# Kernel optimization log

Measured on AMD Instinct MI355X. Metric: run time of the kernel, lower is better.

Reference implementation:

```python
import jax, jax.numpy as jnp
import numpy as np

DT = 0.025    # ms, integration time step
CM = 1.0      # uF/cm^2 membrane capacitance
E_NA, E_K, E_L = 50.0, -77.0, -54.387  # mV reversal potentials

T, N = 8192, 2048


def setup_inputs() -> dict:
    key = jax.random.key(0)
    ks = jax.random.split(key, 5)
    return {
        "input_estim": 5.0 * jax.random.normal(ks[0], (T, N), dtype=jnp.float32),  # uA/cm^2 stim per segment per step
        "V0": -65.0 + 2.0 * jax.random.normal(ks[1], (N,), dtype=jnp.float32),
        "m0": 0.05 + 0.02 * jax.random.uniform(ks[2], (N,), dtype=jnp.float32),
        "h0": 0.60 + 0.05 * jax.random.uniform(ks[3], (N,), dtype=jnp.float32),
        "n0": 0.32 + 0.05 * jax.random.uniform(ks[4], (N,), dtype=jnp.float32),
        "g_na": 120.0 * jnp.ones((N,), jnp.float32),
        "g_k": 36.0 * jnp.ones((N,), jnp.float32),
        "g_l": 0.3 * jnp.ones((N,), jnp.float32),
        "g_ax": 5.0 * jnp.ones((N,), jnp.float32),  # axial coupling conductance between neighbor segments
    }


def _rates(V):
    am = 0.1 * (V + 40.0) / (1.0 - jnp.exp(-(V + 40.0) / 10.0))
    bm = 4.0 * jnp.exp(-(V + 65.0) / 18.0)
    ah = 0.07 * jnp.exp(-(V + 65.0) / 20.0)
    bh = 1.0 / (1.0 + jnp.exp(-(V + 35.0) / 10.0))
    an = 0.01 * (V + 55.0) / (1.0 - jnp.exp(-(V + 55.0) / 10.0))
    bn = 0.125 * jnp.exp(-(V + 65.0) / 80.0)
    return am, bm, ah, bh, an, bn


def reference(input_estim, V0, m0, h0, n0, g_na, g_k, g_l, g_ax):
    def step(state, i_stim):
        V, m, h, n = state
        am, bm, ah, bh, an, bn = _rates(V)
        i_ion = (g_na * m**3 * h * (V - E_NA)
                 + g_k * n**4 * (V - E_K)
                 + g_l * (V - E_L))
        # sealed-end cable: zero-flux boundaries via edge padding
        Vp = jnp.pad(V, (1, 1), mode="edge")
        i_ax = g_ax * (Vp[:-2] + Vp[2:] - 2.0 * V)
        dV = (i_ax + i_stim - i_ion) / CM
        # total transmembrane current (capacitive + ionic) = axial + stim
        mem_cur = CM * dV + i_ion
        new_state = (V + DT * dV,
                     m + DT * (am * (1.0 - m) - bm * m),
                     h + DT * (ah * (1.0 - h) - bh * h),
                     n + DT * (an * (1.0 - n) - bn * n))
        return new_state, (mem_cur, V)

    state0 = (V0, m0, h0, n0)
    (Vf, mf, hf, nf), (mem_currents, mem_voltages) = jax.lax.scan(step, state0, input_estim)
    # (mem_currents_over_time, mem_voltage_over_time, final state)
    return mem_currents, mem_voltages, Vf, mf, hf, nf
```

## Files before the change

### kernel.cpp

```cpp
#include <hip/hip_runtime.h>

typedef unsigned long long u64;
typedef unsigned int u32;

#define TSTEPS 8192
#define NSEG   2048
#define DTC    0.025f

#define KST    28
#define KTAIL  16
#define WAVE   64
#define COWN   8
#define NBLK   (NSEG / COWN)
#define NPH    ((TSTEPS + KST - 1) / KST)
#define JLO    KST
#define LDP    66

constexpr double L2E = 1.4426950408889634074;

#define AM_A ((float)(-0.1 * L2E))
#define CEM  0.018315638888734179f
#define CEH  0.030197383422318501f
#define CEN  0.0040867714384640666f
#define BM_A ((float)(-L2E / 18.0))
#define BM_B ((float)(2.0 - 65.0 * L2E / 18.0))
#define QA   ((float)(-L2E / 80.0))
#define QB   ((float)(-65.0 * L2E / 80.0))
#define CAH  0.2645751311064591f

#define AL(p) __hip_atomic_load((p), __ATOMIC_RELAXED, __HIP_MEMORY_SCOPE_AGENT)
#define AS(p, v) __hip_atomic_store((p), (v), __ATOMIC_RELAXED, __HIP_MEMORY_SCOPE_AGENT)

__device__ __forceinline__ u64 pack_tag(float v, int tag) {
    return ((u64)(u32)tag << 32) | (u64)__float_as_uint(v);
}
__device__ __forceinline__ float lo_f(u64 w) { return __uint_as_float((u32)w); }
__device__ __forceinline__ float bperm(int addr, float v) {
    return __int_as_float(__builtin_amdgcn_ds_bpermute(addr, __float_as_int(v)));
}

__device__ __forceinline__ void rates(float V, float& am, float& bm,
                                      float& ah, float& bh,
                                      float& an, float& bn)
{
    const float em0 = __builtin_amdgcn_exp2f(V * AM_A);
    am = __builtin_fmaf(0.1f, V, 4.0f) *
         __builtin_amdgcn_rcpf(__builtin_fmaf(-CEM, em0, 1.0f));
    an = __builtin_fmaf(0.01f, V, 0.55f) *
         __builtin_amdgcn_rcpf(__builtin_fmaf(-CEN, em0, 1.0f));
    bh = __builtin_amdgcn_rcpf(__builtin_fmaf(CEH, em0, 1.0f));
    bm = __builtin_amdgcn_exp2f(__builtin_fmaf(V, BM_A, BM_B));
    const float q = __builtin_amdgcn_exp2f(__builtin_fmaf(V, QA, QB));
    const float tq = CAH * (q * q);
    ah = tq * tq;
    bn = 0.125f * q;
}

template <int KS>
__device__ __forceinline__ void run_phase(
    int p, int b, int j, int s, int sc,
    bool owned, int addrL, int addrR,
    float gna, float gk, float gl, float gax,
    const float* __restrict__ stim, u64* __restrict__ tstate,
    float* __restrict__ out_cur, float* __restrict__ out_volt,
    float* lds, float& V, float& m, float& h, float& n, bool pub)
{
    const int t0 = p * KST;
    const float* sp = stim + (size_t)t0 * NSEG + sc;

    float st[KS];
#pragma unroll
    for (int k = 0; k < KS; ++k)
        st[k] = sp[(size_t)k * NSEG];
    __builtin_amdgcn_sched_barrier(0);

    const bool needLoad = (!owned) || (p == 0);
    const u64* sb = tstate + (size_t)(p & 1) * 4 * NSEG + sc;
    {
        u64 w0 = 0, w1 = 0, w2 = 0, w3 = 0;
        int ok;
        do {
            ok = 1;
            if (needLoad) {
                w0 = AL(sb);            w1 = AL(sb + NSEG);
                w2 = AL(sb + 2 * NSEG); w3 = AL(sb + 3 * NSEG);
                ok = (int)(w0 >> 32) >= p && (int)(w1 >> 32) >= p &&
                     (int)(w2 >> 32) >= p && (int)(w3 >> 32) >= p;
            }
        } while (!__all(ok));
        if (needLoad) {
            V = lo_f(w0); m = lo_f(w1); h = lo_f(w2); n = lo_f(w3);
        }
    }

    float Vl = bperm(addrL, V);
    float Vr = bperm(addrR, V);
    float am, bm, ah, bh, an, bn;
    rates(V, am, bm, ah, bh, an, bn);

    float2* ld2 = (float2*)lds;
#pragma unroll
    for (int k = 0; k < KS; ++k) {
        const float is = st[k];
        const float ax = (Vl + Vr) - 2.0f * V;
        const float mc = __builtin_fmaf(gax, ax, is);
        const float m3 = m * m * m;
        const float n2 = n * n;
        const float i_ion = gna * m3 * h * (V - 50.0f)
                          + gk * (n2 * n2) * (V + 77.0f)
                          + gl * (V + 54.387f);
        const float dV = mc - i_ion;
        const float Vn = __builtin_fmaf(DTC, dV, V);
        const float VlN = bperm(addrL, Vn);
        const float VrN = bperm(addrR, Vn);

        ld2[k * LDP + j] = make_float2(mc, V);

        float amN, bmN, ahN, bhN, anN, bnN;
        rates(Vn, amN, bmN, ahN, bhN, anN, bnN);

        m = __builtin_fmaf(DTC, __builtin_fmaf(-(am + bm), m, am), m);
        h = __builtin_fmaf(DTC, __builtin_fmaf(-(ah + bh), h, ah), h);
        n = __builtin_fmaf(DTC, __builtin_fmaf(-(an + bn), n, an), n);

        V = Vn; Vl = VlN; Vr = VrN;
        am = amN; bm = bmN; ah = ahN; bh = bhN; an = anN; bn = bnN;
    }

    if (pub && owned) {
        u64* pb = tstate + (size_t)((p + 1) & 1) * 4 * NSEG + s;
        AS(pb,            pack_tag(V, p + 1));
        AS(pb + NSEG,     pack_tag(m, p + 1));
        AS(pb + 2 * NSEG, pack_tag(h, p + 1));
        AS(pb + 3 * NSEG, pack_tag(n, p + 1));
    }
    __builtin_amdgcn_sched_barrier(0);

    const int sbase = b * COWN;
#pragma unroll
    for (int base = 0; base < KS * COWN; base += WAVE) {
        const int idx = base + j;
        if (idx < KS * COWN) {
            const int t  = idx >> 3;
            const int sl = idx & 7;
            const float* lp = lds + (size_t)(t * LDP + JLO + sl) * 2;
            const size_t go = (size_t)(t0 + t) * NSEG + (sbase + sl);
            __builtin_nontemporal_store(lp[0], out_cur + go);
            __builtin_nontemporal_store(lp[1], out_volt + go);
        }
    }
}

__global__ __launch_bounds__(WAVE, 1) void hh_persist(
    const float* __restrict__ stim,
    const float* __restrict__ gna_p, const float* __restrict__ gk_p,
    const float* __restrict__ gl_p,  const float* __restrict__ gax_p,
    u64* __restrict__ tstate,
    float* __restrict__ out_cur, float* __restrict__ out_volt,
    float* __restrict__ tail)
{
    const int j = threadIdx.x;
    const int b = blockIdx.x;
    const int s = b * COWN - KST + j;
    const int sc = s < 0 ? 0 : (s > NSEG - 1 ? NSEG - 1 : s);
    const bool owned = (j >= JLO) && (j < JLO + COWN);

    const int jl = (s <= 0)        ? j : (j > 0  ? j - 1 : 0);
    const int jr = (s >= NSEG - 1) ? j : (j < 63 ? j + 1 : 63);
    const int addrL = jl * 4;
    const int addrR = jr * 4;

    const float gna = gna_p[sc], gk = gk_p[sc], gl = gl_p[sc], gax = gax_p[sc];

    __shared__ float lds[KST * LDP * 2];

    float V = 0.f, m = 0.f, h = 0.f, n = 0.f;

    for (int p = 0; p < NPH - 1; ++p)
        run_phase<KST>(p, b, j, s, sc, owned, addrL, addrR, gna, gk, gl, gax,
                       stim, tstate, out_cur, out_volt, lds, V, m, h, n, true);
    run_phase<KTAIL>(NPH - 1, b, j, s, sc, owned, addrL, addrR, gna, gk, gl, gax,
                     stim, tstate, out_cur, out_volt, lds, V, m, h, n, false);

    if (owned) {
        tail[s] = V; tail[NSEG + s] = m;
        tail[2 * NSEG + s] = h; tail[3 * NSEG + s] = n;
    }
}

__global__ void hh_init(const float* __restrict__ V0, const float* __restrict__ m0,
                        const float* __restrict__ h0, const float* __restrict__ n0,
                        u64* __restrict__ tstate)
{
    const int i = blockIdx.x * blockDim.x + threadIdx.x;
    if (i < NSEG) {
        tstate[i]            = pack_tag(V0[i], 0);
        tstate[NSEG + i]     = pack_tag(m0[i], 0);
        tstate[2 * NSEG + i] = pack_tag(h0[i], 0);
        tstate[3 * NSEG + i] = pack_tag(n0[i], 0);
        u64* b1 = tstate + 4 * NSEG;
        const u64 inv = (u64)(u32)0x80000000u << 32;
        b1[i] = inv; b1[NSEG + i] = inv; b1[2 * NSEG + i] = inv; b1[3 * NSEG + i] = inv;
    }
}

extern "C" void kernel_launch(void* const* d_in, const int* in_sizes, int n_in,
                              void* d_out, int out_size, void* d_ws, size_t ws_size,
                              hipStream_t stream)
{
    const float* stim = (const float*)d_in[0];
    const float* V0   = (const float*)d_in[1];
    const float* m0   = (const float*)d_in[2];
    const float* h0   = (const float*)d_in[3];
    const float* n0   = (const float*)d_in[4];
    const float* gna  = (const float*)d_in[5];
    const float* gk   = (const float*)d_in[6];
    const float* gl   = (const float*)d_in[7];
    const float* gax  = (const float*)d_in[8];

    float* out      = (float*)d_out;
    float* out_cur  = out;
    float* out_volt = out + (size_t)TSTEPS * NSEG;
    float* tail     = out + 2 * (size_t)TSTEPS * NSEG;

    u64* tstate = (u64*)d_ws;

    hipLaunchKernelGGL(hh_init, dim3(8), dim3(256), 0, stream,
                       V0, m0, h0, n0, tstate);
    hipLaunchKernelGGL(hh_persist, dim3(NBLK), dim3(WAVE), 0, stream,
                       stim, gna, gk, gl, gax, tstate,
                       out_cur, out_volt, tail);
}
```

Measured before the change: 1.164 ms.

## Split halo window across two waves coupled by per-step LDS ring exchange

New measurement: 2.317 ms. 1.99x slower.

```diff
diff --git a/kernel.cpp b/kernel.cpp
--- a/kernel.cpp
+++ b/kernel.cpp
@@ -7,14 +7,15 @@
 #define NSEG   2048
 #define DTC    0.025f
 
-#define KST    28
+#define KST    56
 #define KTAIL  16
+#define NT     128
 #define WAVE   64
-#define COWN   8
+#define COWN   16
 #define NBLK   (NSEG / COWN)
-#define NPH    ((TSTEPS + KST - 1) / KST)
-#define JLO    KST
-#define LDP    66
+#define NPH    147
+#define JLO    56
+#define RING   4
 
 constexpr double L2E = 1.4426950408889634074;
 
@@ -30,6 +31,8 @@
 
 #define AL(p) __hip_atomic_load((p), __ATOMIC_RELAXED, __HIP_MEMORY_SCOPE_AGENT)
 #define AS(p, v) __hip_atomic_store((p), (v), __ATOMIC_RELAXED, __HIP_MEMORY_SCOPE_AGENT)
+#define LDSL(p) __hip_atomic_load((p), __ATOMIC_RELAXED, __HIP_MEMORY_SCOPE_WORKGROUP)
+#define LDSS(p, v) __hip_atomic_store((p), (v), __ATOMIC_RELAXED, __HIP_MEMORY_SCOPE_WORKGROUP)
 
 __device__ __forceinline__ u64 pack_tag(float v, int tag) {
     return ((u64)(u32)tag << 32) | (u64)__float_as_uint(v);
@@ -58,14 +61,16 @@
 
 template <int KS>
 __device__ __forceinline__ void run_phase(
-    int p, int b, int j, int s, int sc,
-    bool owned, int addrL, int addrR,
+    int p, int b, int tid, int j, int s, int sc,
+    bool owned, bool edge, bool le, bool re, int addrL, int addrR,
     float gna, float gk, float gl, float gax,
+    u64* ringMe, u64* ringOt,
     const float* __restrict__ stim, u64* __restrict__ tstate,
     float* __restrict__ out_cur, float* __restrict__ out_volt,
-    float* lds, float& V, float& m, float& h, float& n, bool pub)
+    float2* lbuf, float& V, float& m, float& h, float& n, bool pub)
 {
     const int t0 = p * KST;
+    const int g0 = t0;
     const float* sp = stim + (size_t)t0 * NSEG + sc;
 
     float st[KS];
@@ -93,14 +98,28 @@
         }
     }
 
+    if (edge) LDSS(ringMe + (g0 & (RING - 1)), pack_tag(V, g0 + 1));
     float Vl = bperm(addrL, V);
     float Vr = bperm(addrR, V);
+    {
+        u64 w = 0; int ok;
+        do {
+            ok = 1;
+            if (edge) {
+                w = LDSL(ringOt + (g0 & (RING - 1)));
+                ok = (int)(w >> 32) >= g0 + 1;
+            }
+        } while (!__all(ok));
+        if (edge) { if (tid == 63) Vr = lo_f(w); else Vl = lo_f(w); }
+    }
+    Vl = le ? V : Vl;
+    Vr = re ? V : Vr;
     float am, bm, ah, bh, an, bn;
     rates(V, am, bm, ah, bh, an, bn);
 
-    float2* ld2 = (float2*)lds;
 #pragma unroll
     for (int k = 0; k < KS; ++k) {
+        const int G = g0 + k;
         const float is = st[k];
         const float ax = (Vl + Vr) - 2.0f * V;
         const float mc = __builtin_fmaf(gax, ax, is);
@@ -111,10 +130,11 @@
                           + gl * (V + 54.387f);
         const float dV = mc - i_ion;
         const float Vn = __builtin_fmaf(DTC, dV, V);
-        const float VlN = bperm(addrL, Vn);
-        const float VrN = bperm(addrR, Vn);
-
-        ld2[k * LDP + j] = make_float2(mc, V);
+        if (edge) LDSS(ringMe + ((G + 1) & (RING - 1)), pack_tag(Vn, G + 2));
+        float VlN = bperm(addrL, Vn);
+        float VrN = bperm(addrR, Vn);
+
+        if (owned) lbuf[k * 8 + (tid & 7)] = make_float2(mc, V);
 
         float amN, bmN, ahN, bhN, anN, bnN;
         rates(Vn, amN, bmN, ahN, bhN, anN, bnN);
@@ -122,6 +142,20 @@
         m = __builtin_fmaf(DTC, __builtin_fmaf(-(am + bm), m, am), m);
         h = __builtin_fmaf(DTC, __builtin_fmaf(-(ah + bh), h, ah), h);
         n = __builtin_fmaf(DTC, __builtin_fmaf(-(an + bn), n, an), n);
+
+        {
+            u64 w = 0; int ok;
+            do {
+                ok = 1;
+                if (edge) {
+                    w = LDSL(ringOt + ((G + 1) & (RING - 1)));
+                    ok = (int)(w >> 32) >= G + 2;
+                }
+            } while (!__all(ok));
+            if (edge) { if (tid == 63) VrN = lo_f(w); else VlN = lo_f(w); }
+        }
+        VlN = le ? Vn : VlN;
+        VrN = re ? Vn : VrN;
 
         V = Vn; Vl = VlN; Vr = VrN;
         am = amN; bm = bmN; ah = ahN; bh = bhN; an = anN; bn = bnN;
@@ -136,22 +170,20 @@
     }
     __builtin_amdgcn_sched_barrier(0);
 
-    const int sbase = b * COWN;
+    const int sbase = b * COWN + ((tid >= WAVE) ? 8 : 0);
 #pragma unroll
-    for (int base = 0; base < KS * COWN; base += WAVE) {
+    for (int base = 0; base < KS * 8; base += WAVE) {
         const int idx = base + j;
-        if (idx < KS * COWN) {
-            const int t  = idx >> 3;
-            const int sl = idx & 7;
-            const float* lp = lds + (size_t)(t * LDP + JLO + sl) * 2;
-            const size_t go = (size_t)(t0 + t) * NSEG + (sbase + sl);
-            __builtin_nontemporal_store(lp[0], out_cur + go);
-            __builtin_nontemporal_store(lp[1], out_volt + go);
+        if (idx < KS * 8) {
+            const float2 v = lbuf[idx];
+            const size_t go = (size_t)(t0 + (idx >> 3)) * NSEG + sbase + (idx & 7);
+            __builtin_nontemporal_store(v.x, out_cur + go);
+            __builtin_nontemporal_store(v.y, out_volt + go);
         }
     }
 }
 
-__global__ __launch_bounds__(WAVE, 1) void hh_persist(
+__global__ __launch_bounds__(NT, 1) void hh_persist(
     const float* __restrict__ stim,
     const float* __restrict__ gna_p, const float* __restrict__ gk_p,
     const float* __restrict__ gl_p,  const float* __restrict__ gax_p,
@@ -159,28 +191,39 @@
     float* __restrict__ out_cur, float* __restrict__ out_volt,
     float* __restrict__ tail)
 {
-    const int j = threadIdx.x;
-    const int b = blockIdx.x;
-    const int s = b * COWN - KST + j;
-    const int sc = s < 0 ? 0 : (s > NSEG - 1 ? NSEG - 1 : s);
-    const bool owned = (j >= JLO) && (j < JLO + COWN);
-
-    const int jl = (s <= 0)        ? j : (j > 0  ? j - 1 : 0);
-    const int jr = (s >= NSEG - 1) ? j : (j < 63 ? j + 1 : 63);
-    const int addrL = jl * 4;
-    const int addrR = jr * 4;
+    const int tid = threadIdx.x;
+    const int j   = tid & 63;
+    const int b   = blockIdx.x;
+    const int s   = b * COWN - KST + tid;
+    const int sc  = s < 0 ? 0 : (s > NSEG - 1 ? NSEG - 1 : s);
+    const bool owned = (tid >= JLO) && (tid < JLO + COWN);
+    const bool edge  = (tid == 63) || (tid == 64);
+    const bool le = (s <= 0);
+    const bool re = (s >= NSEG - 1);
+
+    const int addrL = (j > 0  ? j - 1 : j) * 4;
+    const int addrR = (j < 63 ? j + 1 : j) * 4;
 
     const float gna = gna_p[sc], gk = gk_p[sc], gl = gl_p[sc], gax = gax_p[sc];
 
-    __shared__ float lds[KST * LDP * 2];
+    __shared__ u64 ring[2][RING];
+    __shared__ float2 lb0[KST * 8], lb1[KST * 8];
+    float2* lbuf = (tid < WAVE) ? lb0 : lb1;
+    u64* ringMe = (tid == 63) ? ring[0] : ring[1];
+    u64* ringOt = (tid == 63) ? ring[1] : ring[0];
+
+    if (tid < 2 * RING) ((u64*)ring)[tid] = 0;
+    __syncthreads();
 
     float V = 0.f, m = 0.f, h = 0.f, n = 0.f;
 
     for (int p = 0; p < NPH - 1; ++p)
-        run_phase<KST>(p, b, j, s, sc, owned, addrL, addrR, gna, gk, gl, gax,
-                       stim, tstate, out_cur, out_volt, lds, V, m, h, n, true);
-    run_phase<KTAIL>(NPH - 1, b, j, s, sc, owned, addrL, addrR, gna, gk, gl, gax,
-                     stim, tstate, out_cur, out_volt, lds, V, m, h, n, false);
+        run_phase<KST>(p, b, tid, j, s, sc, owned, edge, le, re, addrL, addrR,
+                       gna, gk, gl, gax, ringMe, ringOt, stim, tstate,
+                       out_cur, out_volt, lbuf, V, m, h, n, true);
+    run_phase<KTAIL>(NPH - 1, b, tid, j, s, sc, owned, edge, le, re, addrL, addrR,
+                     gna, gk, gl, gax, ringMe, ringOt, stim, tstate,
+                     out_cur, out_volt, lbuf, V, m, h, n, false);
 
     if (owned) {
         tail[s] = V; tail[NSEG + s] = m;
@@ -227,7 +270,7 @@
 
     hipLaunchKernelGGL(hh_init, dim3(8), dim3(256), 0, stream,
                        V0, m0, h0, n0, tstate);
-    hipLaunchKernelGGL(hh_persist, dim3(NBLK), dim3(WAVE), 0, stream,
+    hipLaunchKernelGGL(hh_persist, dim3(NBLK), dim3(NT), 0, stream,
                        stim, gna, gk, gl, gax, tstate,
                        out_cur, out_volt, tail);
 }
```
